# Performance work log

Measured on AMD Instinct MI355X. Metric: run time of the kernel, lower is better.

## Reference

```python
import jax, jax.numpy as jnp
import numpy as np

B, N, C, H, KC, STAGES = 8, 4096, 256, 8, 128, 3
C4 = 4 * C
HD = C4 // H
SCALE = (C // H) ** -0.5  # torch uses head_dim of ORIGINAL dim: (256//8)^-0.5


def _l2norm(x, axis):
    # torch: inp / (1e-6 + inp.norm(dim=axis, keepdim=True))
    return x / (1e-6 + jnp.linalg.norm(x, axis=axis, keepdims=True))


def _dta_branch(xc):
    """EM-style clustering on one stream. xc: [B, 4C, N] -> bases [B, 4C, KC]."""
    b, c, n = xc.shape
    # AdaptiveMaxPool1d(KC): N % KC == 0 -> uniform windows of size N//KC
    bases = _l2norm(xc.reshape(b, c, KC, n // KC).max(axis=-1), axis=1)
    xn = xc.transpose(0, 2, 1)  # [B, N, 4C]
    for _ in range(STAGES):
        z = jax.nn.softmax(jnp.einsum('bnc,bck->bnk', xn, bases), axis=2)  # [B,N,KC]
        z = _l2norm(z, axis=1)
        bases = _l2norm(jnp.einsum('bnc,bnk->bck', xn, z), axis=1)  # [B,4C,KC]
    return bases


def setup_inputs() -> dict:
    key = jax.random.key(0)
    ks = jax.random.split(key, 6)
    x = jax.random.normal(ks[0], (B, N, C), jnp.float32)
    Wq = jax.random.normal(ks[1], (C4, C), jnp.float32) * 0.02
    Wk = jax.random.normal(ks[2], (C4, C), jnp.float32) * 0.02
    Wv = jax.random.normal(ks[3], (C4, C), jnp.float32) * 0.02
    Wp = jax.random.normal(ks[4], (C, C4), jnp.float32) * 0.02
    bp = jnp.zeros((C,), jnp.float32)
    return {"x": x, "Wq": Wq, "Wk": Wk, "Wv": Wv, "Wp": Wp, "bp": bp}


def reference(x, Wq, Wk, Wv, Wp, bp):
    # q/k/v projections (bias-free), [B,N,4C]
    q = x @ Wq.T
    k = x @ Wk.T
    v = x @ Wv.T
    # DTA: note torch does `q, k = self.DA(q, k)` where DA(x1,x2) returns
    # (bases_from_x1, bases_from_x2) -> q bases from q-stream, k bases from k-stream.
    qb = _dta_branch(q.transpose(0, 2, 1))  # [B,4C,KC]
    kb = _dta_branch(k.transpose(0, 2, 1))  # [B,4C,KC]
    qh = qb.reshape(B, H, HD, KC)  # == torch q.permute(0,1,3,2): [B,H,hd,KC]
    kh = kb.reshape(B, H, HD, KC)
    vh = v.transpose(0, 2, 1).reshape(B, H, HD, N)  # [B,H,hd,N]
    # att over cluster axis KC -> [B,H,hd,hd]
    att = jax.nn.softmax(jnp.einsum('bhdk,bhek->bhde', qh, kh) * SCALE, axis=-1)
    o = jnp.einsum('bhde,bhen->bhdn', att, vh)  # [B,H,hd,N]
    # rearrange 'b n_h head_dim n -> b n (n_h head_dim)'
    o = o.transpose(0, 3, 1, 2).reshape(B, N, C4)
    return jax.nn.relu(o @ Wp.T + bp)
```

## Files before the change

### kernel.cpp

```cpp
#include <hip/hip_runtime.h>
#include <hip/hip_bf16.h>

#define NSEQ 4096
#define C4   1024
#define SCALE_F 0.17677669529663687f
#define SLC   524288

typedef __attribute__((ext_vector_type(8))) short bf16x8;
typedef __attribute__((ext_vector_type(4))) float f32x4;
typedef __attribute__((ext_vector_type(8))) unsigned short u16x8;
typedef __attribute__((ext_vector_type(4))) unsigned short u16x4;

__device__ __forceinline__ unsigned short f2b(float x){
  union{float f; unsigned u;} v; v.f = x;
  unsigned r = v.u + 0x7fffu + ((v.u>>16)&1u);
  return (unsigned short)(r>>16);
}
__device__ __forceinline__ unsigned mapf(float x){
  unsigned u = __float_as_uint(x);
  return (u & 0x80000000u) ? ~u : (u | 0x80000000u);
}
__device__ __forceinline__ float unmapf(unsigned m){
  unsigned u = (m & 0x80000000u) ? (m ^ 0x80000000u) : ~m;
  return __uint_as_float(u);
}

typedef __attribute__((address_space(1))) void* gas_p;
typedef __attribute__((address_space(3))) void* las_p;
#define GLDS16(gp, lp) __builtin_amdgcn_global_load_lds((gas_p)(gp), (las_p)(lp), 16, 0, 0)

#define WAITVM8() asm volatile("s_waitcnt vmcnt(8)" ::: "memory")
#define WAITVM4() asm volatile("s_waitcnt vmcnt(4)" ::: "memory")
#define WAITVM0() asm volatile("s_waitcnt vmcnt(0)" ::: "memory")
#define WAITLGKM() asm volatile("s_waitcnt lgkmcnt(0)" ::: "memory")
__device__ __forceinline__ void barrier(){
  asm volatile("" ::: "memory");
  __builtin_amdgcn_s_barrier();
  asm volatile("" ::: "memory");
}

__device__ __forceinline__ void stage128x64s(const unsigned short* G, int row0, int ld, int k0,
                                             unsigned short* lds, int tid){
#pragma unroll
  for (int i = 0; i < 4; ++i){
    int cid = i*256 + tid;
    int r = cid >> 3, c8 = cid & 7;
    GLDS16(G + (row0 + r)*ld + k0 + ((c8 ^ (r & 7))*8), lds + cid*8);
  }
}

template<int LD, int NK, int MA, int MB>
__device__ __forceinline__ void mma_tiles(const unsigned short* ldsA, const unsigned short* ldsB,
                                          f32x4 acc[4][4], int wr, int wc, int lane){
  const int rowg = lane & 15, q4 = lane >> 4;
#pragma unroll
  for (int kc = 0; kc < NK; ++kc){
    bf16x8 a[4], b[4];
#pragma unroll
    for (int mf = 0; mf < 4; ++mf){
      int row = wr*64 + mf*16 + rowg;
      int off;
      if constexpr (MA == 1) off = ((kc*4 + q4) ^ (row & 7)) * 8;
      else                   off = kc*32 + q4*8;
      a[mf] = *(const bf16x8*)(ldsA + row*LD + off);
    }
#pragma unroll
    for (int nf = 0; nf < 4; ++nf){
      int col = wc*64 + nf*16 + rowg;
      int off;
      if constexpr (MB == 1)      off = ((kc*4 + q4) ^ (col & 7)) * 8;
      else if constexpr (MB == 2) off = (kc*32 + q4*8) ^ ((((col>>3) ^ col) & 7) << 3);
      else                        off = kc*32 + q4*8;
      b[nf] = *(const bf16x8*)(ldsB + col*LD + off);
    }
#pragma unroll
    for (int mf = 0; mf < 4; ++mf)
#pragma unroll
      for (int nf = 0; nf < 4; ++nf)
        acc[mf][nf] = __builtin_amdgcn_mfma_f32_16x16x32_bf16(a[mf], b[nf], acc[mf][nf], 0, 0, 0);
  }
}

__global__ __launch_bounds__(256) void k_cast(const float* __restrict__ src,
                                              unsigned short* __restrict__ dst, int n){
  int i = (blockIdx.x*256 + threadIdx.x) * 4;
  if (i < n){
    float4 v = *(const float4*)(src + i);
    u16x4 o = { f2b(v.x), f2b(v.y), f2b(v.z), f2b(v.w) };
    *(u16x4*)(dst + i) = o;
  }
}

__global__ __launch_bounds__(256) void k_wprep(const float* __restrict__ Wq, const float* __restrict__ Wk,
                                               const float* __restrict__ Wv, const float* __restrict__ Wp,
                                               unsigned short* __restrict__ Wcat,
                                               unsigned short* __restrict__ Wpbf,
                                               unsigned short* __restrict__ WcatT,
                                               unsigned short* __restrict__ WvT){
  int t = blockIdx.x*256 + threadIdx.x;
  int s = blockIdx.y;
  if (s < 3){
    const float* src = (s == 0) ? Wq : (s == 1) ? Wk : Wp;
    unsigned short* dst = (s == 0) ? Wcat : (s == 1) ? (Wcat + 262144) : Wpbf;
    int i = t*4;
    float4 v = *(const float4*)(src + i);
    u16x4 o = { f2b(v.x), f2b(v.y), f2b(v.z), f2b(v.w) };
    *(u16x4*)(dst + i) = o;
  } else {
    const float* src = (s == 3) ? Wv : (s == 4) ? Wq : Wk;
    unsigned short* dst = (s == 3) ? WvT : WcatT;
    int ld  = (s == 3) ? 1024 : 2048;
    int off = (s == 5) ? 1024 : 0;
    int j = t & 255, r0 = (t >> 8) * 4;
    u16x4 o = { f2b(src[(r0+0)*256 + j]), f2b(src[(r0+1)*256 + j]),
                f2b(src[(r0+2)*256 + j]), f2b(src[(r0+3)*256 + j]) };
    *(u16x4*)(dst + j*ld + off + r0) = o;
  }
}

__global__ __launch_bounds__(256) void k_gemm_qk(const unsigned short* __restrict__ xbf,
                                                 const unsigned short* __restrict__ Wcat,
                                                 unsigned* __restrict__ pooled){
  __shared__ __align__(16) unsigned short ldsA[128*64];
  __shared__ __align__(16) unsigned short ldsB[128*64];
  int tid = threadIdx.x, lane = tid & 63, wid = tid >> 6, wr = wid >> 1, wc = wid & 1;
  int m0 = blockIdx.x*128, n0 = blockIdx.y*128;
  f32x4 acc[4][4] = {};
  for (int k0 = 0; k0 < 256; k0 += 64){
    __syncthreads();
    stage128x64s(xbf,  m0, 256, k0, ldsA, tid);
    stage128x64s(Wcat, n0, 256, k0, ldsB, tid);
    __syncthreads();
    mma_tiles<64,2,1,1>(ldsA, ldsB, acc, wr, wc, lane);
  }
  int colg = lane & 15;
  int b = m0 >> 12, kbase = (m0 & 4095) >> 5;
#pragma unroll
  for (int nf = 0; nf < 4; ++nf){
    float wlo = -3e38f, whi = -3e38f;
#pragma unroll
    for (int r = 0; r < 4; ++r){
      wlo = fmaxf(wlo, fmaxf(acc[0][nf][r], acc[1][nf][r]));
      whi = fmaxf(whi, fmaxf(acc[2][nf][r], acc[3][nf][r]));
    }
    wlo = fmaxf(wlo, __shfl_xor(wlo, 16)); wlo = fmaxf(wlo, __shfl_xor(wlo, 32));
    whi = fmaxf(whi, __shfl_xor(whi, 16)); whi = fmaxf(whi, __shfl_xor(whi, 32));
    if (lane < 16){
      int col = n0 + wc*64 + nf*16 + colg;
      int sbp = b + ((col >> 10) << 3);
      int c4 = col & 1023;
      atomicMax(&pooled[(sbp*128 + kbase + wr*2    )*C4 + c4], mapf(wlo));
      atomicMax(&pooled[(sbp*128 + kbase + wr*2 + 1)*C4 + c4], mapf(whi));
    }
  }
}

__global__ __launch_bounds__(256) void k_norm(const float* __restrict__ bRaw,
                                              const unsigned* __restrict__ pooled,
                                              unsigned short* __restrict__ basesT, int S){
  int row = blockIdx.x, tid = threadIdx.x, lane = tid & 63, wid = tid >> 6;
  float4 v;
  if (S == 0){
    uint4 u = *(const uint4*)(pooled + row*C4 + tid*4);
    v.x = unmapf(u.x); v.y = unmapf(u.y); v.z = unmapf(u.z); v.w = unmapf(u.w);
  } else {
    v = *(const float4*)(bRaw + row*C4 + tid*4);
  }
  float ss = v.x*v.x + v.y*v.y + v.z*v.z + v.w*v.w;
  __shared__ float red[5];
#pragma unroll
  for (int o = 32; o; o >>= 1) ss += __shfl_down(ss, o);
  if (lane == 0) red[wid] = ss;
  __syncthreads();
  if (tid == 0) red[4] = 1.f / (1e-6f + sqrtf(red[0] + red[1] + red[2] + red[3]));
  __syncthreads();
  float inv = red[4];
  u16x4 o4 = { f2b(v.x*inv), f2b(v.y*inv), f2b(v.z*inv), f2b(v.w*inv) };
  *(u16x4*)(basesT + row*C4 + tid*4) = o4;
}

__global__ __launch_bounds__(256) void k_pb(const unsigned short* __restrict__ basesT,
                                            const unsigned short* __restrict__ WcatT,
                                            unsigned short* __restrict__ PBT){
  __shared__ __align__(16) unsigned short ldsA[2][8192];
  __shared__ __align__(16) unsigned short ldsB[2][8192];
  int tid = threadIdx.x, lane = tid & 63, wid = tid >> 6, wr = wid >> 1, wc = wid & 1;
  int n0 = blockIdx.x*128, sb = blockIdx.y;
  const unsigned short* A = basesT + sb*(128*C4);
  int off = (sb >= 8) ? 1024 : 0;
  f32x4 acc[4][4] = {};
  stage128x64s(A,     0,  C4,   0, ldsA[0], tid);
  stage128x64s(WcatT, n0, 2048, off, ldsB[0], tid);
  for (int t = 0; t < 16; ++t){
    int cur = t & 1;
    if (t < 15){
      stage128x64s(A,     0,  C4,   (t+1)*64, ldsA[cur^1], tid);
      stage128x64s(WcatT, n0, 2048, off + (t+1)*64, ldsB[cur^1], tid);
      WAITVM8();
    } else WAITVM0();
    barrier();
    mma_tiles<64,2,1,1>(ldsA[cur], ldsB[cur], acc, wr, wc, lane);
    WAITLGKM();
    barrier();
  }
  int colg = lane & 15, rowg = (lane >> 4) * 4;
#pragma unroll
  for (int mf = 0; mf < 4; ++mf)
#pragma unroll
    for (int nf = 0; nf < 4; ++nf)
#pragma unroll
      for (int r = 0; r < 4; ++r)
        PBT[(sb*128 + wr*64 + mf*16 + rowg + r)*256 + n0 + wc*64 + nf*16 + colg]
          = f2b(acc[mf][nf][r]);
}

__global__ __launch_bounds__(256) void k_gemm_z(const unsigned short* __restrict__ xbf,
                                                const unsigned short* __restrict__ PBT,
                                                unsigned short* __restrict__ zT){
  __shared__ __align__(16) unsigned short smem[32768];
  __shared__ float redb[2][2][128];
  unsigned short* zt = smem;
  int tid = threadIdx.x, lane = tid & 63, wid = tid >> 6, wr = wid >> 1, wc = wid & 1;
  int m0 = blockIdx.x*128, sb = blockIdx.y;
  const unsigned short* A = xbf + (sb & 7)*(NSEQ*256);
  const unsigned short* B = PBT + sb*(128*256);
  f32x4 acc[4][4] = {};
  stage128x64s(A, m0, 256, 0, smem, tid);
  stage128x64s(B, 0,  256, 0, smem + 16384, tid);
  for (int t = 0; t < 4; ++t){
    int cur = t & 1;
    if (t < 3){
      stage128x64s(A, m0, 256, (t+1)*64, smem + (cur^1)*8192, tid);
      stage128x64s(B, 0,  256, (t+1)*64, smem + 16384 + (cur^1)*8192, tid);
      WAITVM8();
    } else WAITVM0();
    barrier();
    mma_tiles<64,2,1,1>(smem + cur*8192, smem + 16384 + cur*8192, acc, wr, wc, lane);
    WAITLGKM();
    barrier();
  }
  int colg = lane & 15, rowg = (lane >> 4) * 4;
  float sm[4][4];
#pragma unroll
  for (int mf = 0; mf < 4; ++mf)
#pragma unroll
    for (int r = 0; r < 4; ++r){
      float m = fmaxf(fmaxf(acc[mf][0][r], acc[mf][1][r]), fmaxf(acc[mf][2][r], acc[mf][3][r]));
#pragma unroll
      for (int o = 1; o < 16; o <<= 1) m = fmaxf(m, __shfl_xor(m, o));
      if (colg == 0) redb[0][wc][wr*64 + mf*16 + rowg + r] = m;
    }
  barrier();
#pragma unroll
  for (int mf = 0; mf < 4; ++mf)
#pragma unroll
    for (int r = 0; r < 4; ++r){
      int idx = wr*64 + mf*16 + rowg + r;
      float m = fmaxf(redb[0][0][idx], redb[0][1][idx]);
      float s = 0.f;
#pragma unroll
      for (int nf = 0; nf < 4; ++nf){
        float e = __expf(acc[mf][nf][r] - m);
        acc[mf][nf][r] = e; s += e;
      }
#pragma unroll
      for (int o = 1; o < 16; o <<= 1) s += __shfl_xor(s, o);
      if (colg == 0) redb[1][wc][idx] = s;
    }
  barrier();
#pragma unroll
  for (int mf = 0; mf < 4; ++mf)
#pragma unroll
    for (int r = 0; r < 4; ++r){
      int idx = wr*64 + mf*16 + rowg + r;
      sm[mf][r] = 1.f / (redb[1][0][idx] + redb[1][1][idx]);
    }
#pragma unroll
  for (int mf = 0; mf < 4; ++mf)
#pragma unroll
    for (int nf = 0; nf < 4; ++nf){
      int k = wc*64 + nf*16 + colg;
      int swz = (k & 7) << 3;
#pragma unroll
      for (int r = 0; r < 4; ++r){
        int n = wr*64 + mf*16 + rowg + r;
        zt[k*128 + (n ^ swz)] = f2b(acc[mf][nf][r] * sm[mf][r]);
      }
    }
  WAITLGKM();
  barrier();
#pragma unroll
  for (int i = 0; i < 8; ++i){
    int cid = i*256 + tid;
    int kk = cid >> 4, j8 = cid & 15;
    int nbase = (j8*8) ^ ((kk & 7) << 3);
    *(uint4*)(zT + sb*(128*NSEQ) + kk*NSEQ + m0 + nbase) = *(const uint4*)(zt + kk*128 + j8*8);
  }
}

__global__ __launch_bounds__(256) void k_gemm_gt(const unsigned short* __restrict__ xbf,
                                                 const unsigned short* __restrict__ zT,
                                                 float* __restrict__ part){
  __shared__ __align__(16) unsigned short ldsA[2][8192];
  __shared__ __align__(16) unsigned short ldsB[2][8192];
  int tid = threadIdx.x, lane = tid & 63, wid = tid >> 6, wr = wid >> 1, wc = wid & 1;
  int c0 = blockIdx.x*128, sb = blockIdx.y, ks = blockIdx.z;
  const unsigned short* xb = xbf + (sb & 7)*(NSEQ*256);
  const unsigned short* Zt = zT + sb*(128*NSEQ);
  int base = ks*512;
  f32x4 acc[4][4] = {};
  u16x8 vB[4];
  int np_[4], c8_[4];
#pragma unroll
  for (int i = 0; i < 4; ++i){
    int cid = i*256 + tid;
    np_[i] = cid >> 4; c8_[i] = cid & 15;
  }
  stage128x64s(Zt, 0, NSEQ, base, ldsA[0], tid);
#pragma unroll
  for (int i = 0; i < 4; ++i)
    vB[i] = *(const u16x8*)(xb + (base + np_[i])*256 + c0 + c8_[i]*8);
  for (int t = 0; t < 8; ++t){
    int cur = t & 1, n0 = base + t*64;
    if (t < 7){
      stage128x64s(Zt, 0, NSEQ, n0 + 64, ldsA[cur^1], tid);
      WAITVM4();
    } else WAITVM0();
#pragma unroll
    for (int i = 0; i < 4; ++i){
#pragma unroll
      for (int j = 0; j < 8; ++j)
        ldsB[cur][(c8_[i]*8 + j)*64 + (np_[i] ^ (((c8_[i] ^ j) & 7) << 3))] = vB[i][j];
    }
    WAITLGKM();
    barrier();
    if (t < 7){
#pragma unroll
      for (int i = 0; i < 4; ++i)
        vB[i] = *(const u16x8*)(xb + (n0 + 64 + np_[i])*256 + c0 + c8_[i]*8);
    }
    mma_tiles<64,2,1,2>(ldsA[cur], ldsB[cur], acc, wr, wc, lane);
    WAITLGKM();
    barrier();
  }
  int colg = lane & 15, rowg = (lane >> 4) * 4;
#pragma unroll
  for (int mf = 0; mf < 4; ++mf)
#pragma unroll
    for (int nf = 0; nf < 4; ++nf)
#pragma unroll
      for (int r = 0; r < 4; ++r)
        part[ks*SLC + (sb*128 + wr*64 + mf*16 + rowg + r)*256 + c0 + wc*64 + nf*16 + colg]
          = acc[mf][nf][r];
}

__global__ __launch_bounds__(256) void k_redgt(const float* __restrict__ src,
                                               unsigned short* __restrict__ dst, int S){
  int i = (blockIdx.x*256 + threadIdx.x) * 4;
  float4 a = {0.f,0.f,0.f,0.f};
  for (int s = 0; s < S; ++s){
    float4 u = *(const float4*)(src + s*SLC + i);
    a.x += u.x; a.y += u.y; a.z += u.z; a.w += u.w;
  }
  u16x4 o = { f2b(a.x), f2b(a.y), f2b(a.z), f2b(a.w) };
  *(u16x4*)(dst + i) = o;
}

__global__ __launch_bounds__(256) void k_pbases(const unsigned short* __restrict__ Wcat,
                                                const unsigned short* __restrict__ GTbf,
                                                float* __restrict__ bRaw){
  __shared__ __align__(16) unsigned short ldsA[128*64];
  __shared__ __align__(16) unsigned short ldsB[128*64];
  int tid = threadIdx.x, lane = tid & 63, wid = tid >> 6, wr = wid >> 1, wc = wid & 1;
  int m0 = blockIdx.x*128, sb = blockIdx.y;
  const unsigned short* A = Wcat + ((sb >= 8) ? 1024*256 : 0);
  const unsigned short* B = GTbf + sb*(128*256);
  f32x4 acc[4][4] = {};
  for (int t = 0; t < 4; ++t){
    __syncthreads();
    stage128x64s(A, m0, 256, t*64, ldsA, tid);
    stage128x64s(B, 0,  256, t*64, ldsB, tid);
    __syncthreads();
    mma_tiles<64,2,1,1>(ldsA, ldsB, acc, wr, wc, lane);
  }
  int colg = lane & 15, rowg = (lane >> 4) * 4;
#pragma unroll
  for (int mf = 0; mf < 4; ++mf)
#pragma unroll
    for (int nf = 0; nf < 4; ++nf)
#pragma unroll
      for (int r = 0; r < 4; ++r){
        int c4 = m0 + wr*64 + mf*16 + rowg + r;
        int k  = wc*64 + nf*16 + colg;
        bRaw[(sb*128 + k)*C4 + c4] = acc[mf][nf][r];
      }
}

__global__ __launch_bounds__(256) void k_attn(const unsigned short* __restrict__ basesT,
                                              unsigned short* __restrict__ attT){
  __shared__ __align__(16) char smem[98816];
  unsigned short* Qlt = (unsigned short*)smem;
  unsigned short* Klt = (unsigned short*)(smem + 32768);
  float* scores       = (float*)smem;
  unsigned short* at  = (unsigned short*)(smem + 66048);
  int tid = threadIdx.x, lane = tid & 63, wid = tid >> 6, wr = wid >> 1, wc = wid & 1;
  int b = blockIdx.x >> 3, h = blockIdx.x & 7;
  const unsigned short* Q = basesT + b*(128*C4) + h*128;
  const unsigned short* K = basesT + (8 + b)*(128*C4) + h*128;
#pragma unroll
  for (int i = 0; i < 8; ++i){
    int cid = i*256 + tid, kk = cid >> 4, c8 = cid & 15;
    u16x8 vq = *(const u16x8*)(Q + kk*C4 + c8*8);
    u16x8 vk = *(const u16x8*)(K + kk*C4 + c8*8);
#pragma unroll
    for (int j = 0; j < 8; ++j){
      Qlt[(c8*8 + j)*128 + kk] = vq[j];
      Klt[(c8*8 + j)*128 + kk] = vk[j];
    }
  }
  __syncthreads();
  f32x4 acc[4][4] = {};
  mma_tiles<128,4,0,0>(Qlt, Klt, acc, wr, wc, lane);
  __syncthreads();
  int colg = lane & 15, rowg = (lane >> 4) * 4;
#pragma unroll
  for (int mf = 0; mf < 4; ++mf)
#pragma unroll
    for (int nf = 0; nf < 4; ++nf)
#pragma unroll
      for (int r = 0; r < 4; ++r)
        scores[(wr*64 + mf*16 + rowg + r)*129 + wc*64 + nf*16 + colg] = acc[mf][nf][r] * SCALE_F;
  __syncthreads();
  if (tid < 128){
    float mx = -3e38f;
    for (int j = 0; j < 128; ++j) mx = fmaxf(mx, scores[tid*129 + j]);
    float s = 0.f;
    for (int j = 0; j < 128; ++j){ float e = __expf(scores[tid*129 + j] - mx); scores[tid*129 + j] = e; s += e; }
    float inv = 1.f / s;
    for (int j = 0; j < 128; ++j) at[j*128 + tid] = f2b(scores[tid*129 + j] * inv);
  }
  __syncthreads();
#pragma unroll
  for (int i = 0; i < 8; ++i){
    int cid = i*256 + tid;
    *(uint4*)(attT + blockIdx.x*16384 + cid*8) = *(const uint4*)(at + cid*8);
  }
}

__global__ __launch_bounds__(256) void k_wpeff(const unsigned short* __restrict__ Wpbf,
                                               const unsigned short* __restrict__ attT,
                                               unsigned short* __restrict__ WpEff){
  __shared__ __align__(16) unsigned short ldsA[128*64];
  __shared__ __align__(16) unsigned short ldsB[128*64];
  int tid = threadIdx.x, lane = tid & 63, wid = tid >> 6, wr = wid >> 1, wc = wid & 1;
  int m0 = blockIdx.x*128;
  int bh = blockIdx.y, b = bh >> 3, h = bh & 7;
  const unsigned short* At = attT + bh*16384;
  f32x4 acc[4][4] = {};
  for (int k0 = 0; k0 < 128; k0 += 64){
    __syncthreads();
    stage128x64s(Wpbf, m0, C4, h*128 + k0, ldsA, tid);
    stage128x64s(At,   0,  128, k0, ldsB, tid);
    __syncthreads();
    mma_tiles<64,2,1,1>(ldsA, ldsB, acc, wr, wc, lane);
  }
  int colg = lane & 15, rowg = (lane >> 4) * 4;
#pragma unroll
  for (int mf = 0; mf < 4; ++mf)
#pragma unroll
    for (int nf = 0; nf < 4; ++nf)
#pragma unroll
      for (int r = 0; r < 4; ++r){
        int row = m0 + wr*64 + mf*16 + rowg + r;
        int col = wc*64 + nf*16 + colg;
        WpEff[b*(256*C4) + row*C4 + h*128 + col] = f2b(acc[mf][nf][r]);
      }
}

__global__ __launch_bounds__(256) void k_gemm_w2(const unsigned short* __restrict__ WpEff,
                                                 const unsigned short* __restrict__ WvT,
                                                 unsigned short* __restrict__ W2){
  __shared__ __align__(16) unsigned short ldsA[128*64];
  __shared__ __align__(16) unsigned short ldsB[128*64];
  int tid = threadIdx.x, lane = tid & 63, wid = tid >> 6, wr = wid >> 1, wc = wid & 1;
  int m0 = blockIdx.x*128, n0 = blockIdx.y*128, b = blockIdx.z;
  const unsigned short* A = WpEff + b*(256*C4);
  f32x4 acc[4][4] = {};
  for (int k0 = 0; k0 < C4; k0 += 64){
    __syncthreads();
    stage128x64s(A,   m0, C4, k0, ldsA, tid);
    stage128x64s(WvT, n0, C4, k0, ldsB, tid);
    __syncthreads();
    mma_tiles<64,2,1,1>(ldsA, ldsB, acc, wr, wc, lane);
  }
  int colg = lane & 15, rowg = (lane >> 4) * 4;
#pragma unroll
  for (int mf = 0; mf < 4; ++mf)
#pragma unroll
    for (int nf = 0; nf < 4; ++nf)
#pragma unroll
      for (int r = 0; r < 4; ++r){
        int row = m0 + wr*64 + mf*16 + rowg + r;
        int col = n0 + wc*64 + nf*16 + colg;
        W2[b*65536 + row*256 + col] = f2b(acc[mf][nf][r]);
      }
}

__global__ __launch_bounds__(256) void k_gemm_out(const unsigned short* __restrict__ xbf,
                                                  const unsigned short* __restrict__ W2,
                                                  const float* __restrict__ bp,
                                                  float* __restrict__ out){
  __shared__ __align__(16) unsigned short ldsA[2][8192];
  __shared__ __align__(16) unsigned short ldsB[2][8192];
  int tid = threadIdx.x, lane = tid & 63, wid = tid >> 6, wr = wid >> 1, wc = wid & 1;
  int m0 = blockIdx.x*128, n0 = blockIdx.y*128, b = blockIdx.z;
  const unsigned short* A = xbf + b*(NSEQ*256);
  const unsigned short* Bm = W2 + b*65536;
  f32x4 acc[4][4] = {};
  stage128x64s(A,  m0, 256, 0, ldsA[0], tid);
  stage128x64s(Bm, n0, 256, 0, ldsB[0], tid);
  for (int t = 0; t < 4; ++t){
    int cur = t & 1;
    if (t < 3){
      stage128x64s(A,  m0, 256, (t+1)*64, ldsA[cur^1], tid);
      stage128x64s(Bm, n0, 256, (t+1)*64, ldsB[cur^1], tid);
      WAITVM8();
    } else WAITVM0();
    barrier();
    mma_tiles<64,2,1,1>(ldsA[cur], ldsB[cur], acc, wr, wc, lane);
    WAITLGKM();
    barrier();
  }
  int colg = lane & 15, rowg = (lane >> 4) * 4;
#pragma unroll
  for (int mf = 0; mf < 4; ++mf)
#pragma unroll
    for (int nf = 0; nf < 4; ++nf){
      int col = n0 + wc*64 + nf*16 + colg;
      float bias = bp[col];
#pragma unroll
      for (int r = 0; r < 4; ++r){
        int row = m0 + wr*64 + mf*16 + rowg + r;
        out[(b*NSEQ + row)*256 + col] = fmaxf(acc[mf][nf][r] + bias, 0.f);
      }
    }
}

extern "C" void kernel_launch(void* const* d_in, const int* in_sizes, int n_in,
                              void* d_out, int out_size, void* d_ws, size_t ws_size,
                              hipStream_t stream){
  (void)in_sizes; (void)n_in; (void)out_size; (void)ws_size;
  const float* x  = (const float*)d_in[0];
  const float* Wq = (const float*)d_in[1];
  const float* Wk = (const float*)d_in[2];
  const float* Wv = (const float*)d_in[3];
  const float* Wp = (const float*)d_in[4];
  const float* bp = (const float*)d_in[5];
  float* out = (float*)d_out;
  char* ws = (char*)d_ws;

  unsigned short* xbf    = (unsigned short*)(ws + 0);
  unsigned short* zT     = (unsigned short*)(ws + 16777216);
  float*          bPart  = (float*)(ws + 33554432);
  unsigned*       pooled = (unsigned*)(ws + 50331648);
  float*          bRawP  = (float*)(ws + 58720256);
  unsigned short* basesT = (unsigned short*)(ws + 67108864);
  unsigned short* WpEff  = (unsigned short*)(ws + 71303168);
  unsigned short* attT   = (unsigned short*)(ws + 75497472);
  unsigned short* PBT    = (unsigned short*)(ws + 77594624);
  unsigned short* GTbf   = (unsigned short*)(ws + 78643200);
  unsigned short* Wcat   = (unsigned short*)(ws + 79691776);
  unsigned short* WcatT  = (unsigned short*)(ws + 80740352);
  unsigned short* W2     = (unsigned short*)(ws + 81788928);
  unsigned short* WvT    = (unsigned short*)(ws + 82837504);
  unsigned short* Wpbf   = (unsigned short*)(ws + 83361792);

  k_cast<<<8192, 256, 0, stream>>>(x, xbf, 8388608);
  k_wprep<<<dim3(256, 6), 256, 0, stream>>>(Wq, Wk, Wv, Wp, Wcat, Wpbf, WcatT, WvT);

  (void)hipMemsetAsync(pooled, 0, (size_t)16*128*1024*4, stream);
  k_gemm_qk<<<dim3(256, 16), 256, 0, stream>>>(xbf, Wcat, pooled);
  k_norm<<<2048, 256, 0, stream>>>(bRawP, pooled, basesT, 0);

  for (int st = 0; st < 3; ++st){
    k_pb<<<dim3(2, 16), 256, 0, stream>>>(basesT, WcatT, PBT);
    k_gemm_z<<<dim3(32, 16), 256, 0, stream>>>(xbf, PBT, zT);
    k_gemm_gt<<<dim3(2, 16, 8), 256, 0, stream>>>(xbf, zT, bPart);
    k_redgt<<<512, 256, 0, stream>>>(bPart, GTbf, 8);
    k_pbases<<<dim3(8, 16), 256, 0, stream>>>(Wcat, GTbf, bRawP);
    k_norm<<<2048, 256, 0, stream>>>(bRawP, pooled, basesT, 1);
  }

  k_attn<<<64, 256, 0, stream>>>(basesT, attT);
  k_wpeff<<<dim3(2, 64), 256, 0, stream>>>(Wpbf, attT, WpEff);
  k_gemm_w2<<<dim3(2, 2, 8), 256, 0, stream>>>(WpEff, WvT, W2);
  k_gemm_out<<<dim3(32, 2, 8), 256, 0, stream>>>(xbf, W2, bp, out);
}
```

Baseline: 315.5 us.

## Split-K the PB GEMM, fuse attention with WpEff, fold pooled memset into cast

The k_pb GEMM, which launched only 32 blocks over K=1024, now splits K four ways into fp32 partials, and an extra k_redgt launch reduces them to bf16. This raises parallelism on a small-grid stage inside the three-stage loop at the cost of an extra reduction kernel and partial-buffer traffic. The attention softmax kernel is fused with the WpEff GEMM, so attT is no longer written and reread. That fused kernel now runs on 128 blocks, which recomputes attention twice per (b,h). The pooled-buffer memset is folded into k_cast to remove one launch.

```diff
diff --git a/kernel.cpp b/kernel.cpp
--- a/kernel.cpp
+++ b/kernel.cpp
@@ -49,6 +49,16 @@
   }
 }
 
+__device__ __forceinline__ void stage128x128s(const unsigned short* G, int row0, int ld, int k0,
+                                              unsigned short* lds, int tid){
+#pragma unroll
+  for (int i = 0; i < 8; ++i){
+    int cid = i*256 + tid;
+    int r = cid >> 4, c16 = cid & 15;
+    GLDS16(G + (row0 + r)*ld + k0 + ((c16 ^ (r & 7))*8), lds + cid*8);
+  }
+}
+
 template<int LD, int NK, int MA, int MB>
 __device__ __forceinline__ void mma_tiles(const unsigned short* ldsA, const unsigned short* ldsB,
                                           f32x4 acc[4][4], int wr, int wc, int lane){
@@ -82,12 +92,17 @@
 }
 
 __global__ __launch_bounds__(256) void k_cast(const float* __restrict__ src,
-                                              unsigned short* __restrict__ dst, int n){
+                                              unsigned short* __restrict__ dst,
+                                              unsigned* __restrict__ pooled, int n){
   int i = (blockIdx.x*256 + threadIdx.x) * 4;
   if (i < n){
     float4 v = *(const float4*)(src + i);
     u16x4 o = { f2b(v.x), f2b(v.y), f2b(v.z), f2b(v.w) };
     *(u16x4*)(dst + i) = o;
+  }
+  if (blockIdx.x < 2048){
+    uint4 z = {0u, 0u, 0u, 0u};
+    *(uint4*)(pooled + (blockIdx.x*256 + threadIdx.x)*4) = z;
   }
 }
 
@@ -181,27 +196,20 @@
 
 __global__ __launch_bounds__(256) void k_pb(const unsigned short* __restrict__ basesT,
                                             const unsigned short* __restrict__ WcatT,
-                                            unsigned short* __restrict__ PBT){
-  __shared__ __align__(16) unsigned short ldsA[2][8192];
-  __shared__ __align__(16) unsigned short ldsB[2][8192];
-  int tid = threadIdx.x, lane = tid & 63, wid = tid >> 6, wr = wid >> 1, wc = wid & 1;
-  int n0 = blockIdx.x*128, sb = blockIdx.y;
+                                            float* __restrict__ part){
+  __shared__ __align__(16) unsigned short ldsA[128*64];
+  __shared__ __align__(16) unsigned short ldsB[128*64];
+  int tid = threadIdx.x, lane = tid & 63, wid = tid >> 6, wr = wid >> 1, wc = wid & 1;
+  int n0 = blockIdx.x*128, sb = blockIdx.y, ks = blockIdx.z;
   const unsigned short* A = basesT + sb*(128*C4);
   int off = (sb >= 8) ? 1024 : 0;
   f32x4 acc[4][4] = {};
-  stage128x64s(A,     0,  C4,   0, ldsA[0], tid);
-  stage128x64s(WcatT, n0, 2048, off, ldsB[0], tid);
-  for (int t = 0; t < 16; ++t){
-    int cur = t & 1;
-    if (t < 15){
-      stage128x64s(A,     0,  C4,   (t+1)*64, ldsA[cur^1], tid);
-      stage128x64s(WcatT, n0, 2048, off + (t+1)*64, ldsB[cur^1], tid);
-      WAITVM8();
-    } else WAITVM0();
-    barrier();
-    mma_tiles<64,2,1,1>(ldsA[cur], ldsB[cur], acc, wr, wc, lane);
-    WAITLGKM();
-    barrier();
+  for (int t = 0; t < 4; ++t){
+    __syncthreads();
+    stage128x64s(A,     0,  C4,   ks*256 + t*64, ldsA, tid);
+    stage128x64s(WcatT, n0, 2048, off + ks*256 + t*64, ldsB, tid);
+    __syncthreads();
+    mma_tiles<64,2,1,1>(ldsA, ldsB, acc, wr, wc, lane);
   }
   int colg = lane & 15, rowg = (lane >> 4) * 4;
 #pragma unroll
@@ -210,8 +218,20 @@
     for (int nf = 0; nf < 4; ++nf)
 #pragma unroll
       for (int r = 0; r < 4; ++r)
-        PBT[(sb*128 + wr*64 + mf*16 + rowg + r)*256 + n0 + wc*64 + nf*16 + colg]
-          = f2b(acc[mf][nf][r]);
+        part[ks*SLC + (sb*128 + wr*64 + mf*16 + rowg + r)*256 + n0 + wc*64 + nf*16 + colg]
+          = acc[mf][nf][r];
+}
+
+__global__ __launch_bounds__(256) void k_redgt(const float* __restrict__ src,
+                                               unsigned short* __restrict__ dst, int S){
+  int i = (blockIdx.x*256 + threadIdx.x) * 4;
+  float4 a = {0.f,0.f,0.f,0.f};
+  for (int s = 0; s < S; ++s){
+    float4 u = *(const float4*)(src + s*SLC + i);
+    a.x += u.x; a.y += u.y; a.z += u.z; a.w += u.w;
+  }
+  u16x4 o = { f2b(a.x), f2b(a.y), f2b(a.z), f2b(a.w) };
+  *(u16x4*)(dst + i) = o;
 }
 
 __global__ __launch_bounds__(256) void k_gemm_z(const unsigned short* __restrict__ xbf,
@@ -354,18 +374,6 @@
           = acc[mf][nf][r];
 }
 
-__global__ __launch_bounds__(256) void k_redgt(const float* __restrict__ src,
-                                               unsigned short* __restrict__ dst, int S){
-  int i = (blockIdx.x*256 + threadIdx.x) * 4;
-  float4 a = {0.f,0.f,0.f,0.f};
-  for (int s = 0; s < S; ++s){
-    float4 u = *(const float4*)(src + s*SLC + i);
-    a.x += u.x; a.y += u.y; a.z += u.z; a.w += u.w;
-  }
-  u16x4 o = { f2b(a.x), f2b(a.y), f2b(a.z), f2b(a.w) };
-  *(u16x4*)(dst + i) = o;
-}
-
 __global__ __launch_bounds__(256) void k_pbases(const unsigned short* __restrict__ Wcat,
                                                 const unsigned short* __restrict__ GTbf,
                                                 float* __restrict__ bRaw){
@@ -396,15 +404,18 @@
       }
 }
 
-__global__ __launch_bounds__(256) void k_attn(const unsigned short* __restrict__ basesT,
-                                              unsigned short* __restrict__ attT){
+__global__ __launch_bounds__(256) void k_attnwp(const unsigned short* __restrict__ basesT,
+                                                const unsigned short* __restrict__ Wpbf,
+                                                unsigned short* __restrict__ WpEff){
   __shared__ __align__(16) char smem[98816];
   unsigned short* Qlt = (unsigned short*)smem;
   unsigned short* Klt = (unsigned short*)(smem + 32768);
   float* scores       = (float*)smem;
   unsigned short* at  = (unsigned short*)(smem + 66048);
-  int tid = threadIdx.x, lane = tid & 63, wid = tid >> 6, wr = wid >> 1, wc = wid & 1;
-  int b = blockIdx.x >> 3, h = blockIdx.x & 7;
+  unsigned short* Wl  = (unsigned short*)smem;
+  int tid = threadIdx.x, lane = tid & 63, wid = tid >> 6, wr = wid >> 1, wc = wid & 1;
+  int m0 = blockIdx.x*128;
+  int bh = blockIdx.y, b = bh >> 3, h = bh & 7;
   const unsigned short* Q = basesT + b*(128*C4) + h*128;
   const unsigned short* K = basesT + (8 + b)*(128*C4) + h*128;
 #pragma unroll
@@ -440,31 +451,10 @@
     for (int j = 0; j < 128; ++j) at[j*128 + tid] = f2b(scores[tid*129 + j] * inv);
   }
   __syncthreads();
-#pragma unroll
-  for (int i = 0; i < 8; ++i){
-    int cid = i*256 + tid;
-    *(uint4*)(attT + blockIdx.x*16384 + cid*8) = *(const uint4*)(at + cid*8);
-  }
-}
-
-__global__ __launch_bounds__(256) void k_wpeff(const unsigned short* __restrict__ Wpbf,
-                                               const unsigned short* __restrict__ attT,
-                                               unsigned short* __restrict__ WpEff){
-  __shared__ __align__(16) unsigned short ldsA[128*64];
-  __shared__ __align__(16) unsigned short ldsB[128*64];
-  int tid = threadIdx.x, lane = tid & 63, wid = tid >> 6, wr = wid >> 1, wc = wid & 1;
-  int m0 = blockIdx.x*128;
-  int bh = blockIdx.y, b = bh >> 3, h = bh & 7;
-  const unsigned short* At = attT + bh*16384;
-  f32x4 acc[4][4] = {};
-  for (int k0 = 0; k0 < 128; k0 += 64){
-    __syncthreads();
-    stage128x64s(Wpbf, m0, C4, h*128 + k0, ldsA, tid);
-    stage128x64s(At,   0,  128, k0, ldsB, tid);
-    __syncthreads();
-    mma_tiles<64,2,1,1>(ldsA, ldsB, acc, wr, wc, lane);
-  }
-  int colg = lane & 15, rowg = (lane >> 4) * 4;
+  stage128x128s(Wpbf, m0, C4, h*128, Wl, tid);
+  __syncthreads();
+  f32x4 acc2[4][4] = {};
+  mma_tiles<128,4,1,0>(Wl, at, acc2, wr, wc, lane);
 #pragma unroll
   for (int mf = 0; mf < 4; ++mf)
 #pragma unroll
@@ -473,7 +463,7 @@
       for (int r = 0; r < 4; ++r){
         int row = m0 + wr*64 + mf*16 + rowg + r;
         int col = wc*64 + nf*16 + colg;
-        WpEff[b*(256*C4) + row*C4 + h*128 + col] = f2b(acc[mf][nf][r]);
+        WpEff[b*(256*C4) + row*C4 + h*128 + col] = f2b(acc2[mf][nf][r]);
       }
 }
 
@@ -566,7 +556,6 @@
   float*          bRawP  = (float*)(ws + 58720256);
   unsigned short* basesT = (unsigned short*)(ws + 67108864);
   unsigned short* WpEff  = (unsigned short*)(ws + 71303168);
-  unsigned short* attT   = (unsigned short*)(ws + 75497472);
   unsigned short* PBT    = (unsigned short*)(ws + 77594624);
   unsigned short* GTbf   = (unsigned short*)(ws + 78643200);
   unsigned short* Wcat   = (unsigned short*)(ws + 79691776);
@@ -575,15 +564,15 @@
   unsigned short* WvT    = (unsigned short*)(ws + 82837504);
   unsigned short* Wpbf   = (unsigned short*)(ws + 83361792);
 
-  k_cast<<<8192, 256, 0, stream>>>(x, xbf, 8388608);
+  k_cast<<<8192, 256, 0, stream>>>(x, xbf, pooled, 8388608);
   k_wprep<<<dim3(256, 6), 256, 0, stream>>>(Wq, Wk, Wv, Wp, Wcat, Wpbf, WcatT, WvT);
 
-  (void)hipMemsetAsync(pooled, 0, (size_t)16*128*1024*4, stream);
   k_gemm_qk<<<dim3(256, 16), 256, 0, stream>>>(xbf, Wcat, pooled);
   k_norm<<<2048, 256, 0, stream>>>(bRawP, pooled, basesT, 0);
 
   for (int st = 0; st < 3; ++st){
-    k_pb<<<dim3(2, 16), 256, 0, stream>>>(basesT, WcatT, PBT);
+    k_pb<<<dim3(2, 16, 4), 256, 0, stream>>>(basesT, WcatT, bPart);
+    k_redgt<<<512, 256, 0, stream>>>(bPart, PBT, 4);
     k_gemm_z<<<dim3(32, 16), 256, 0, stream>>>(xbf, PBT, zT);
     k_gemm_gt<<<dim3(2, 16, 8), 256, 0, stream>>>(xbf, zT, bPart);
     k_redgt<<<512, 256, 0, stream>>>(bPart, GTbf, 8);
@@ -591,8 +580,7 @@
     k_norm<<<2048, 256, 0, stream>>>(bRawP, pooled, basesT, 1);
   }
 
-  k_attn<<<64, 256, 0, stream>>>(basesT, attT);
-  k_wpeff<<<dim3(2, 64), 256, 0, stream>>>(Wpbf, attT, WpEff);
+  k_attnwp<<<dim3(2, 64), 256, 0, stream>>>(basesT, Wpbf, WpEff);
   k_gemm_w2<<<dim3(2, 2, 8), 256, 0, stream>>>(WpEff, WvT, W2);
   k_gemm_out<<<dim3(32, 2, 8), 256, 0, stream>>>(xbf, W2, bp, out);
 }
```

After: 288.9 us, median of 3. -8.4%, faster.
